# Kernel tuning notes

Measured on AMD Instinct MI355X. Metric: run time of the kernel, lower is better.

Reference implementation:

```python
import jax, jax.numpy as jnp
import numpy as np

H = 1024  # hidden_size
IN = 1024  # input_size
EPS = 1e-05


def _ln(v):
    # LayerNorm over last dim, no affine (gamma/beta applied by caller)
    c = v - v.mean(-1, keepdims=True)
    return c * jax.lax.rsqrt((c * c).mean(-1, keepdims=True) + EPS)


def setup_inputs() -> dict:
    key = jax.random.key(0)
    ks = jax.random.split(key, 12)
    stdv = 1.0 / np.sqrt(IN + 2 * H)
    u = lambda k, shape, s=stdv: jax.random.uniform(k, shape, jnp.float32, -s, s)
    bias = jnp.zeros((4 * H,), jnp.float32).at[:H].set(1.0)
    return {
        "input": jax.random.normal(ks[0], (512, 64, IN), jnp.float32),
        "hidden": jax.random.normal(ks[1], (64, H), jnp.float32),
        "cell": jax.random.normal(ks[2], (64, H), jnp.float32),
        "weight_ih": u(ks[3], (4 * H, IN)),
        "weight_hh": u(ks[4], (4 * H, H)),
        "weight_ch": u(ks[5], (3 * H,)),
        "bias": bias,
        "gamma_f": jax.random.uniform(ks[6], (H,), jnp.float32),
        "gamma_i": jax.random.uniform(ks[7], (H,), jnp.float32),
        "gamma_g": jax.random.uniform(ks[8], (H,), jnp.float32),
        "gamma_o": jax.random.uniform(ks[9], (H,), jnp.float32),
        "gamma_cell": jax.random.uniform(ks[10], (H,), jnp.float32),
        "beta_cell": jnp.zeros((H,), jnp.float32),
    }


def reference(input, hidden, cell, weight_ih, weight_hh, weight_ch, bias,
              gamma_f, gamma_i, gamma_g, gamma_o, gamma_cell, beta_cell):
    # input: [T, B, IN]; hidden/cell: [B, H]. Eval mode (dropout inactive).
    w_cf, w_ci, w_co = weight_ch[:H], weight_ch[H:2 * H], weight_ch[2 * H:]
    b_f, b_i, b_g, b_o = jnp.split(bias, 4)
    # Precompute input projections for all timesteps: [T, B, 4H]
    x_proj = jnp.einsum('tbi,gi->tbg', input, weight_ih)

    def step(carry, xp):
        h, c = carry
        gates = xp + h @ weight_hh.T  # [B, 4H]
        f_hat, i_hat, g_hat, o_hat = jnp.split(gates, 4, axis=-1)
        f = jax.nn.sigmoid(_ln(f_hat + w_cf * c) * gamma_f + b_f)
        i = jax.nn.sigmoid(_ln(i_hat + w_ci * c) * gamma_i + b_i)
        g = jnp.tanh(_ln(g_hat) * gamma_g + b_g)
        c_new = f * c + i * g
        c_ln = _ln(c_new) * gamma_cell + beta_cell
        o = jax.nn.sigmoid(_ln(o_hat + w_co * c_new) * gamma_o + b_o)
        h_new = o * jnp.tanh(c_ln)
        return (h_new, c_new), h_new

    (h_f, c_f), out = jax.lax.scan(step, (hidden, cell), x_proj)
    return out, h_f, c_f
```

## Files before the change

### kernel.cpp

```cpp
#include <hip/hip_runtime.h>

#define T_STEPS 512
#define BATCH   64
#define HID     1024
#define GDIM    4096
#define KDIM    2048
#define NGW     128
#define NSW     64
#define CWG     32
#define BHID    (BATCH * HID)

using short8  = __attribute__((ext_vector_type(8))) short;
using floatx4 = __attribute__((ext_vector_type(4))) float;
typedef unsigned long long u64;

__device__ inline unsigned short bf16_rne(float f) {
  union { float f; unsigned u; } x; x.f = f;
  unsigned r = x.u + 0x7FFFu + ((x.u >> 16) & 1u);
  return (unsigned short)(r >> 16);
}

__device__ inline float sigmoid_(float x) { return 1.0f / (1.0f + __expf(-x)); }
__device__ inline float tanh_(float x) {
  float e = __expf(-2.0f * fabsf(x));
  float r = (1.0f - e) / (1.0f + e);
  return copysignf(r, x);
}

#define LOAD4(dst, ptr) { float4 _t4 = *(const float4*)(ptr); \
  dst[0]=_t4.x; dst[1]=_t4.y; dst[2]=_t4.z; dst[3]=_t4.w; }

__device__ inline u64 ld_u64_mall(const void* p) {
  return __hip_atomic_load((const u64*)p, __ATOMIC_RELAXED, __HIP_MEMORY_SCOPE_AGENT);
}
__device__ inline void st_u64_mall(void* p, u64 v) {
  __hip_atomic_store((u64*)p, v, __ATOMIC_RELAXED, __HIP_MEMORY_SCOPE_AGENT);
}
__device__ inline void st_u32_mall(void* p, unsigned v) {
  __hip_atomic_store((unsigned*)p, v, __ATOMIC_RELAXED, __HIP_MEMORY_SCOPE_AGENT);
}
__device__ inline unsigned ld_u32_mall(const void* p) {
  return __hip_atomic_load((const unsigned*)p, __ATOMIC_RELAXED, __HIP_MEMORY_SCOPE_AGENT);
}
__device__ inline short8 ld_a16_mall(const unsigned short* p) {
  union { u64 q[2]; short8 v; } u;
  u.q[0] = ld_u64_mall(p);
  u.q[1] = ld_u64_mall(p + 4);
  return u.v;
}
__device__ inline void ld4f_mall(float* d, const float* p) {
  union { u64 q; float f[2]; } a, b;
  a.q = ld_u64_mall(p);
  b.q = ld_u64_mall(p + 2);
  d[0] = a.f[0]; d[1] = a.f[1]; d[2] = b.f[0]; d[3] = b.f[1];
}
__device__ inline void st4h_mall(unsigned short* p, float a, float b, float c, float d) {
  union { u64 q; unsigned short s[4]; } u;
  u.s[0] = bf16_rne(a); u.s[1] = bf16_rne(b); u.s[2] = bf16_rne(c); u.s[3] = bf16_rne(d);
  st_u64_mall(p, u.q);
}

__global__ __launch_bounds__(256) void cvt_w_kernel(
    const float* __restrict__ w_hh, const float* __restrict__ w_ih,
    unsigned short* __restrict__ wcat)
{
  int idx  = blockIdx.x * 256 + threadIdx.x;
  int base = idx * 4;
  int g = base >> 11;
  int k = base & 2047;
  const float* src = (k < 1024) ? (w_hh + (size_t)g * 1024 + k)
                                : (w_ih + (size_t)g * 1024 + (k - 1024));
  float a = src[0], b = src[1], c = src[2], d = src[3];
  uint2 v;
  v.x = (unsigned)bf16_rne(a) | ((unsigned)bf16_rne(b) << 16);
  v.y = (unsigned)bf16_rne(c) | ((unsigned)bf16_rne(d) << 16);
  *(uint2*)(wcat + base) = v;
}

__global__ __launch_bounds__(256) void cvt_x_kernel(
    const float* __restrict__ x, unsigned short* __restrict__ xall)
{
  size_t i = ((size_t)blockIdx.x * 256 + threadIdx.x) * 8;
  float4 a = *(const float4*)(x + i);
  float4 b = *(const float4*)(x + i + 4);
  union { unsigned short s[8]; uint4 v; } u;
  u.s[0] = bf16_rne(a.x); u.s[1] = bf16_rne(a.y); u.s[2] = bf16_rne(a.z); u.s[3] = bf16_rne(a.w);
  u.s[4] = bf16_rne(b.x); u.s[5] = bf16_rne(b.y); u.s[6] = bf16_rne(b.z); u.s[7] = bf16_rne(b.w);
  *(uint4*)(xall + i) = u.v;
}

__global__ __launch_bounds__(256) void init_kernel(
    const float* __restrict__ hidden, const float* __restrict__ x0,
    const float* __restrict__ cell,
    unsigned short* __restrict__ hdst, unsigned short* __restrict__ xdst,
    float* __restrict__ c_ws)
{
  const int b = blockIdx.x;
  const int j = threadIdx.x * 4;
  const size_t off = (size_t)b * HID + j;
  float4 h = *(const float4*)(hidden + off);
  float4 x = *(const float4*)(x0 + off);
  float4 c = *(const float4*)(cell + off);
  ushort4 hv, xv;
  hv.x = bf16_rne(h.x); hv.y = bf16_rne(h.y); hv.z = bf16_rne(h.z); hv.w = bf16_rne(h.w);
  xv.x = bf16_rne(x.x); xv.y = bf16_rne(x.y); xv.z = bf16_rne(x.z); xv.w = bf16_rne(x.w);
  *(ushort4*)(hdst + off) = hv;
  *(ushort4*)(xdst + off) = xv;
  *(float4*)(c_ws + off) = c;
}

template<int N>
__device__ inline void block_reduce(float* v, float* red, int tid) {
#pragma unroll
  for (int i = 0; i < N; ++i) {
    float x = v[i];
#pragma unroll
    for (int off = 32; off > 0; off >>= 1)
      x += __shfl_xor(x, off, 64);
    v[i] = x;
  }
  const int wave = tid >> 6;
  if ((tid & 63) == 0) {
#pragma unroll
    for (int i = 0; i < N; ++i) red[wave * N + i] = v[i];
  }
  __syncthreads();
#pragma unroll
  for (int i = 0; i < N; ++i)
    v[i] = red[i] + red[N + i] + red[2 * N + i] + red[3 * N + i];
}

#define MFMA16(a, b, c) __builtin_amdgcn_mfma_f32_16x16x32_bf16(a, b, c, 0, 0, 0)

template<int XALL>
__global__ __launch_bounds__(256, 1) void lstm_persist(
    const unsigned short* __restrict__ wcat,
    const float* __restrict__ input,
    const unsigned short* __restrict__ xA,
    unsigned short* __restrict__ xbuf,
    float* __restrict__ gates, float* __restrict__ c_ws,
    const float* __restrict__ w_ch, const float* __restrict__ bias,
    const float* __restrict__ gamma_f, const float* __restrict__ gamma_i,
    const float* __restrict__ gamma_g, const float* __restrict__ gamma_o,
    const float* __restrict__ gamma_c, const float* __restrict__ beta_c,
    float* __restrict__ out,
    unsigned short* __restrict__ hbuf,
    unsigned* __restrict__ syncp)
{
  __shared__ __align__(16) unsigned short smB[CWG * KDIM];
  __shared__ float sm[40];

  const int wg   = blockIdx.x;
  const int tid  = threadIdx.x;
  const int wave = tid >> 6;
  const int lane = tid & 63;
  const int quad = lane >> 4;
  const int l16  = lane & 15;

  unsigned* gflags = syncp;
  unsigned* hflags = syncp + NGW * 16;

  const floatx4 z = {0.f, 0.f, 0.f, 0.f};

  if (wg < NGW) {
    const int n0 = wg * CWG;
    for (int i = 0; i < 32; ++i) {
      int idx = wave * 32 + i;
      int t2 = idx >> 6, kc = idx & 63;
      short8 v = *(const short8*)(wcat + (size_t)(n0 + t2 * 16 + l16) * KDIM
                                  + kc * 32 + quad * 8);
      *(short8*)(smB + (size_t)idx * 512 + lane * 8) = v;
    }
    __syncthreads();

    const size_t rowoff = (size_t)(wave * 16 + l16) * HID + quad * 8;

    for (int t = 0; t < T_STEPS; ++t) {
      floatx4 x0e = z, x1e = z, x0o = z, x1o = z;
      if (XALL) {
        const unsigned short* ax = xA + (size_t)t * BHID + rowoff;
#pragma unroll
        for (int kc = 0; kc < 32; kc += 2) {
          short8 ae  = *(const short8*)(ax + kc * 32);
          short8 ao  = *(const short8*)(ax + (kc + 1) * 32);
          short8 b0e = *(const short8*)(smB + (size_t)(32 + kc) * 512 + lane * 8);
          short8 b1e = *(const short8*)(smB + (size_t)(96 + kc) * 512 + lane * 8);
          short8 b0o = *(const short8*)(smB + (size_t)(33 + kc) * 512 + lane * 8);
          short8 b1o = *(const short8*)(smB + (size_t)(97 + kc) * 512 + lane * 8);
          x0e = MFMA16(ae, b0e, x0e); x1e = MFMA16(ae, b1e, x1e);
          x0o = MFMA16(ao, b0o, x0o); x1o = MFMA16(ao, b1o, x1o);
        }
      }

      if (tid < NSW) {
        const unsigned* fp = hflags + tid * 16;
        while (ld_u32_mall(fp) < (unsigned)t) { }
      }
      __syncthreads();

      if (!XALL) {
#pragma unroll
        for (int kc = 0; kc < 32; kc += 2) {
          short8 ae  = ld_a16_mall(xA + rowoff + kc * 32);
          short8 ao  = ld_a16_mall(xA + rowoff + (kc + 1) * 32);
          short8 b0e = *(const short8*)(smB + (size_t)(32 + kc) * 512 + lane * 8);
          short8 b1e = *(const short8*)(smB + (size_t)(96 + kc) * 512 + lane * 8);
          short8 b0o = *(const short8*)(smB + (size_t)(33 + kc) * 512 + lane * 8);
          short8 b1o = *(const short8*)(smB + (size_t)(97 + kc) * 512 + lane * 8);
          x0e = MFMA16(ae, b0e, x0e); x1e = MFMA16(ae, b1e, x1e);
          x0o = MFMA16(ao, b0o, x0o); x1o = MFMA16(ao, b1o, x1o);
        }
      }

      short8 aH[32];
#pragma unroll
      for (int kc = 0; kc < 32; ++kc)
        aH[kc] = ld_a16_mall(hbuf + rowoff + kc * 32);

      floatx4 h0e = z, h1e = z, h0o = z, h1o = z;
#pragma unroll
      for (int kc = 0; kc < 32; kc += 2) {
        short8 b0e = *(const short8*)(smB + (size_t)kc * 512 + lane * 8);
        short8 b1e = *(const short8*)(smB + (size_t)(64 + kc) * 512 + lane * 8);
        short8 b0o = *(const short8*)(smB + (size_t)(kc + 1) * 512 + lane * 8);
        short8 b1o = *(const short8*)(smB + (size_t)(65 + kc) * 512 + lane * 8);
        h0e = MFMA16(aH[kc],     b0e, h0e); h1e = MFMA16(aH[kc],     b1e, h1e);
        h0o = MFMA16(aH[kc + 1], b0o, h0o); h1o = MFMA16(aH[kc + 1], b1o, h1o);
      }

#pragma unroll
      for (int r = 0; r < 4; ++r) {
        int m = wave * 16 + quad * 4 + r;
        float* gm = gates + (size_t)m * GDIM + n0 + l16;
        st_u32_mall(gm,      __float_as_uint((h0e[r] + h0o[r]) + (x0e[r] + x0o[r])));
        st_u32_mall(gm + 16, __float_as_uint((h1e[r] + h1o[r]) + (x1e[r] + x1o[r])));
      }
      asm volatile("s_waitcnt vmcnt(0)" ::: "memory");
      __syncthreads();
      if (tid == 0)
        st_u32_mall(gflags + wg * 16, (unsigned)(t + 1));
    }
  } else {
    const int b = wg - NGW;
    const int j = tid * 4;

    float cc[4], wcf[4], wci[4], wco[4];
    float gf4[4], gi4[4], gg4[4], go4[4], gc4[4], bc4[4];
    float bf4[4], bi4[4], bg4[4], bo4[4];
    LOAD4(cc,  c_ws + (size_t)b * HID + j);
    LOAD4(wcf, w_ch + j);
    LOAD4(wci, w_ch + HID + j);
    LOAD4(wco, w_ch + 2 * HID + j);
    LOAD4(gf4, gamma_f + j); LOAD4(gi4, gamma_i + j);
    LOAD4(gg4, gamma_g + j); LOAD4(go4, gamma_o + j);
    LOAD4(gc4, gamma_c + j); LOAD4(bc4, beta_c + j);
    LOAD4(bf4, bias + j);           LOAD4(bi4, bias + HID + j);
    LOAD4(bg4, bias + 2 * HID + j); LOAD4(bo4, bias + 3 * HID + j);
    const float invH = 1.0f / (float)HID;

    for (int t = 0; t < T_STEPS; ++t) {
      const int has_next = (t + 1 < T_STEPS);
      float4 xv;
      if (!XALL && has_next)
        xv = *(const float4*)(input + (size_t)(t + 1) * BHID + (size_t)b * HID + j);

      if (tid < NGW) {
        const unsigned* fp = gflags + tid * 16;
        while (ld_u32_mall(fp) < (unsigned)(t + 1)) { }
      }
      __syncthreads();

      float fh[4], ih[4], gh[4], oh[4];
      const float* grow = gates + (size_t)b * GDIM;
      ld4f_mall(fh, grow + j);
      ld4f_mall(ih, grow + HID + j);
      ld4f_mall(gh, grow + 2 * HID + j);
      ld4f_mall(oh, grow + 3 * HID + j);

      if (!XALL && has_next)
        st4h_mall(xbuf + (size_t)b * HID + j, xv.x, xv.y, xv.z, xv.w);

      float af[4], ai[4], ag[4];
      float s[6] = {0, 0, 0, 0, 0, 0};
#pragma unroll
      for (int r = 0; r < 4; ++r) {
        af[r] = fh[r] + wcf[r] * cc[r];
        ai[r] = ih[r] + wci[r] * cc[r];
        ag[r] = gh[r];
        s[0] += af[r]; s[1] += af[r] * af[r];
        s[2] += ai[r]; s[3] += ai[r] * ai[r];
        s[4] += ag[r]; s[5] += ag[r] * ag[r];
      }
      block_reduce<6>(s, sm, tid);
      float mu_f = s[0] * invH, is_f = rsqrtf(s[1] * invH - mu_f * mu_f + 1e-5f);
      float mu_i = s[2] * invH, is_i = rsqrtf(s[3] * invH - mu_i * mu_i + 1e-5f);
      float mu_g = s[4] * invH, is_g = rsqrtf(s[5] * invH - mu_g * mu_g + 1e-5f);

      float cn[4], ao[4];
      float s2[4] = {0, 0, 0, 0};
#pragma unroll
      for (int r = 0; r < 4; ++r) {
        float f = sigmoid_((af[r] - mu_f) * is_f * gf4[r] + bf4[r]);
        float i = sigmoid_((ai[r] - mu_i) * is_i * gi4[r] + bi4[r]);
        float g = tanh_((ag[r] - mu_g) * is_g * gg4[r] + bg4[r]);
        cn[r] = f * cc[r] + i * g;
        ao[r] = oh[r] + wco[r] * cn[r];
        s2[0] += cn[r]; s2[1] += cn[r] * cn[r];
        s2[2] += ao[r]; s2[3] += ao[r] * ao[r];
      }
#pragma unroll
      for (int r = 0; r < 4; ++r) cc[r] = cn[r];

      block_reduce<4>(s2, sm + 24, tid);
      float mu_c = s2[0] * invH, is_c = rsqrtf(s2[1] * invH - mu_c * mu_c + 1e-5f);
      float mu_o = s2[2] * invH, is_o = rsqrtf(s2[3] * invH - mu_o * mu_o + 1e-5f);

      float h4[4];
#pragma unroll
      for (int r = 0; r < 4; ++r) {
        float cl = (cn[r] - mu_c) * is_c * gc4[r] + bc4[r];
        float o  = sigmoid_((ao[r] - mu_o) * is_o * go4[r] + bo4[r]);
        h4[r] = o * tanh_(cl);
      }
      { float4 tt; tt.x = h4[0]; tt.y = h4[1]; tt.z = h4[2]; tt.w = h4[3];
        *(float4*)(out + (size_t)t * BHID + (size_t)b * HID + j) = tt; }
      st4h_mall(hbuf + (size_t)b * HID + j, h4[0], h4[1], h4[2], h4[3]);

      asm volatile("s_waitcnt vmcnt(0)" ::: "memory");
      __syncthreads();
      if (tid == 0)
        st_u32_mall(hflags + b * 16, (unsigned)(t + 1));
    }

    { float4 tt; tt.x = cc[0]; tt.y = cc[1]; tt.z = cc[2]; tt.w = cc[3];
      *(float4*)(c_ws + (size_t)b * HID + j) = tt; }
  }
}

extern "C" void kernel_launch(void* const* d_in, const int* in_sizes, int n_in,
                              void* d_out, int out_size, void* d_ws, size_t ws_size,
                              hipStream_t stream) {
  (void)in_sizes; (void)n_in; (void)out_size;
  const float* input   = (const float*)d_in[0];
  const float* hidden  = (const float*)d_in[1];
  const float* cell    = (const float*)d_in[2];
  const float* w_ih    = (const float*)d_in[3];
  const float* w_hh    = (const float*)d_in[4];
  const float* w_ch    = (const float*)d_in[5];
  const float* bias    = (const float*)d_in[6];
  const float* gamma_f = (const float*)d_in[7];
  const float* gamma_i = (const float*)d_in[8];
  const float* gamma_g = (const float*)d_in[9];
  const float* gamma_o = (const float*)d_in[10];
  const float* gamma_c = (const float*)d_in[11];
  const float* beta_c  = (const float*)d_in[12];
  float* out = (float*)d_out;

  const size_t SZ_WCAT = (size_t)GDIM * KDIM * sizeof(unsigned short);
  const size_t SZ_XALL = (size_t)T_STEPS * BHID * sizeof(unsigned short);
  const size_t SZ_BUF  = (size_t)BHID * sizeof(unsigned short);
  const size_t SZ_GATE = (size_t)BATCH * GDIM * sizeof(float);
  const size_t SZ_VEC  = (size_t)BHID * sizeof(float);
  const size_t SZ_FLAG = 16384;
  const size_t NEED_XALL = SZ_WCAT + SZ_XALL + SZ_BUF + SZ_GATE + SZ_VEC + SZ_FLAG;

  char* p = (char*)d_ws;
  unsigned short* wcat = (unsigned short*)p;  p += SZ_WCAT;
  const int xall = (ws_size >= NEED_XALL) ? 1 : 0;

  unsigned short *xA, *xbuf;
  if (xall) { xA = (unsigned short*)p; p += SZ_XALL; xbuf = xA; }
  else      { xA = (unsigned short*)p; p += SZ_BUF;  xbuf = xA; }
  unsigned short* hbuf = (unsigned short*)p;  p += SZ_BUF;
  float* gates = (float*)p;  p += SZ_GATE;
  float* c_ws  = (float*)p;  p += SZ_VEC;
  unsigned* syncp = (unsigned*)p;

  cvt_w_kernel<<<(GDIM * KDIM / 4) / 256, 256, 0, stream>>>(w_hh, w_ih, wcat);
  if (xall)
    cvt_x_kernel<<<((size_t)T_STEPS * BHID / 8) / 256, 256, 0, stream>>>(input, xA);
  init_kernel<<<BATCH, 256, 0, stream>>>(hidden, input, cell, hbuf, xA, c_ws);
  hipMemsetAsync(syncp, 0, SZ_FLAG, stream);

  if (xall)
    lstm_persist<1><<<NGW + NSW, 256, 0, stream>>>(
        wcat, input, xA, xbuf, gates, c_ws, w_ch, bias, gamma_f, gamma_i,
        gamma_g, gamma_o, gamma_c, beta_c, out, hbuf, syncp);
  else
    lstm_persist<0><<<NGW + NSW, 256, 0, stream>>>(
        wcat, input, xA, xbuf, gates, c_ws, w_ch, bias, gamma_f, gamma_i,
        gamma_g, gamma_o, gamma_c, beta_c, out, hbuf, syncp);

  const size_t OUT0 = (size_t)T_STEPS * BHID;
  hipMemcpyAsync(out + OUT0, out + (OUT0 - BHID),
                 (size_t)BHID * sizeof(float), hipMemcpyDeviceToDevice, stream);
  hipMemcpyAsync(out + OUT0 + BHID, c_ws,
                 (size_t)BHID * sizeof(float), hipMemcpyDeviceToDevice, stream);
}
```

Before: 7.245 ms.

## Use per-timestep hidden-state buffer pool and pack sync flags densely

Adds a mode where each timestep's bf16 hidden state goes to its own slot in a T-long pool, so the gate workgroups read h with ordinary cached loads instead of MALL-bypass loads. Reusing a single buffer forced uncached loads to avoid stale data. The sync flags are also packed contiguously instead of one per 64 bytes, which changes how the flag polling hits cache lines. The new mode needs extra workspace and falls back to the old modes when it is not available.

```diff
diff --git a/kernel.cpp b/kernel.cpp
--- a/kernel.cpp
+++ b/kernel.cpp
@@ -132,7 +132,7 @@
 
 #define MFMA16(a, b, c) __builtin_amdgcn_mfma_f32_16x16x32_bf16(a, b, c, 0, 0, 0)
 
-template<int XALL>
+template<int MODE>
 __global__ __launch_bounds__(256, 1) void lstm_persist(
     const unsigned short* __restrict__ wcat,
     const float* __restrict__ input,
@@ -144,7 +144,7 @@
     const float* __restrict__ gamma_g, const float* __restrict__ gamma_o,
     const float* __restrict__ gamma_c, const float* __restrict__ beta_c,
     float* __restrict__ out,
-    unsigned short* __restrict__ hbuf,
+    unsigned short* __restrict__ hA,
     unsigned* __restrict__ syncp)
 {
   __shared__ __align__(16) unsigned short smB[CWG * KDIM];
@@ -158,7 +158,7 @@
   const int l16  = lane & 15;
 
   unsigned* gflags = syncp;
-  unsigned* hflags = syncp + NGW * 16;
+  unsigned* hflags = syncp + 512;
 
   const floatx4 z = {0.f, 0.f, 0.f, 0.f};
 
@@ -177,7 +177,7 @@
 
     for (int t = 0; t < T_STEPS; ++t) {
       floatx4 x0e = z, x1e = z, x0o = z, x1o = z;
-      if (XALL) {
+      if (MODE >= 1) {
         const unsigned short* ax = xA + (size_t)t * BHID + rowoff;
 #pragma unroll
         for (int kc = 0; kc < 32; kc += 2) {
@@ -193,12 +193,12 @@
       }
 
       if (tid < NSW) {
-        const unsigned* fp = hflags + tid * 16;
+        const unsigned* fp = hflags + tid;
         while (ld_u32_mall(fp) < (unsigned)t) { }
       }
       __syncthreads();
 
-      if (!XALL) {
+      if (MODE == 0) {
 #pragma unroll
         for (int kc = 0; kc < 32; kc += 2) {
           short8 ae  = ld_a16_mall(xA + rowoff + kc * 32);
@@ -213,9 +213,16 @@
       }
 
       short8 aH[32];
-#pragma unroll
-      for (int kc = 0; kc < 32; ++kc)
-        aH[kc] = ld_a16_mall(hbuf + rowoff + kc * 32);
+      if (MODE == 2) {
+        const unsigned short* ah = hA + (size_t)t * BHID + rowoff;
+#pragma unroll
+        for (int kc = 0; kc < 32; ++kc)
+          aH[kc] = *(const short8*)(ah + kc * 32);
+      } else {
+#pragma unroll
+        for (int kc = 0; kc < 32; ++kc)
+          aH[kc] = ld_a16_mall(hA + rowoff + kc * 32);
+      }
 
       floatx4 h0e = z, h1e = z, h0o = z, h1o = z;
 #pragma unroll
@@ -238,7 +245,7 @@
       asm volatile("s_waitcnt vmcnt(0)" ::: "memory");
       __syncthreads();
       if (tid == 0)
-        st_u32_mall(gflags + wg * 16, (unsigned)(t + 1));
+        st_u32_mall(gflags + wg, (unsigned)(t + 1));
     }
   } else {
     const int b = wg - NGW;
@@ -261,11 +268,11 @@
     for (int t = 0; t < T_STEPS; ++t) {
       const int has_next = (t + 1 < T_STEPS);
       float4 xv;
-      if (!XALL && has_next)
+      if (MODE == 0 && has_next)
         xv = *(const float4*)(input + (size_t)(t + 1) * BHID + (size_t)b * HID + j);
 
       if (tid < NGW) {
-        const unsigned* fp = gflags + tid * 16;
+        const unsigned* fp = gflags + tid;
         while (ld_u32_mall(fp) < (unsigned)(t + 1)) { }
       }
       __syncthreads();
@@ -277,7 +284,7 @@
       ld4f_mall(gh, grow + 2 * HID + j);
       ld4f_mall(oh, grow + 3 * HID + j);
 
-      if (!XALL && has_next)
+      if (MODE == 0 && has_next)
         st4h_mall(xbuf + (size_t)b * HID + j, xv.x, xv.y, xv.z, xv.w);
 
       float af[4], ai[4], ag[4];
@@ -324,12 +331,17 @@
       }
       { float4 tt; tt.x = h4[0]; tt.y = h4[1]; tt.z = h4[2]; tt.w = h4[3];
         *(float4*)(out + (size_t)t * BHID + (size_t)b * HID + j) = tt; }
-      st4h_mall(hbuf + (size_t)b * HID + j, h4[0], h4[1], h4[2], h4[3]);
+      if (has_next) {
+        unsigned short* hd = (MODE == 2)
+            ? hA + (size_t)(t + 1) * BHID + (size_t)b * HID + j
+            : hA + (size_t)b * HID + j;
+        st4h_mall(hd, h4[0], h4[1], h4[2], h4[3]);
+      }
 
       asm volatile("s_waitcnt vmcnt(0)" ::: "memory");
       __syncthreads();
       if (tid == 0)
-        st_u32_mall(hflags + b * 16, (unsigned)(t + 1));
+        st_u32_mall(hflags + b, (unsigned)(t + 1));
     }
 
     { float4 tt; tt.x = cc[0]; tt.y = cc[1]; tt.z = cc[2]; tt.w = cc[3];
@@ -358,38 +370,49 @@
 
   const size_t SZ_WCAT = (size_t)GDIM * KDIM * sizeof(unsigned short);
   const size_t SZ_XALL = (size_t)T_STEPS * BHID * sizeof(unsigned short);
+  const size_t SZ_HPOOL= (size_t)T_STEPS * BHID * sizeof(unsigned short);
   const size_t SZ_BUF  = (size_t)BHID * sizeof(unsigned short);
   const size_t SZ_GATE = (size_t)BATCH * GDIM * sizeof(float);
   const size_t SZ_VEC  = (size_t)BHID * sizeof(float);
   const size_t SZ_FLAG = 16384;
-  const size_t NEED_XALL = SZ_WCAT + SZ_XALL + SZ_BUF + SZ_GATE + SZ_VEC + SZ_FLAG;
+  const size_t TAIL = SZ_GATE + SZ_VEC + SZ_FLAG;
+  const size_t NEED2 = SZ_WCAT + SZ_XALL + SZ_HPOOL + TAIL;
+  const size_t NEED1 = SZ_WCAT + SZ_XALL + SZ_BUF + TAIL;
 
   char* p = (char*)d_ws;
   unsigned short* wcat = (unsigned short*)p;  p += SZ_WCAT;
-  const int xall = (ws_size >= NEED_XALL) ? 1 : 0;
-
-  unsigned short *xA, *xbuf;
-  if (xall) { xA = (unsigned short*)p; p += SZ_XALL; xbuf = xA; }
-  else      { xA = (unsigned short*)p; p += SZ_BUF;  xbuf = xA; }
-  unsigned short* hbuf = (unsigned short*)p;  p += SZ_BUF;
+  int mode = (ws_size >= NEED2) ? 2 : (ws_size >= NEED1) ? 1 : 0;
+
+  unsigned short *xA, *xbuf, *hA;
+  if (mode >= 1) {
+    xA = (unsigned short*)p; p += SZ_XALL; xbuf = xA;
+    hA = (unsigned short*)p; p += (mode == 2) ? SZ_HPOOL : SZ_BUF;
+  } else {
+    xA = (unsigned short*)p; p += SZ_BUF;  xbuf = xA;
+    hA = (unsigned short*)p; p += SZ_BUF;
+  }
   float* gates = (float*)p;  p += SZ_GATE;
   float* c_ws  = (float*)p;  p += SZ_VEC;
   unsigned* syncp = (unsigned*)p;
 
   cvt_w_kernel<<<(GDIM * KDIM / 4) / 256, 256, 0, stream>>>(w_hh, w_ih, wcat);
-  if (xall)
+  if (mode >= 1)
     cvt_x_kernel<<<((size_t)T_STEPS * BHID / 8) / 256, 256, 0, stream>>>(input, xA);
-  init_kernel<<<BATCH, 256, 0, stream>>>(hidden, input, cell, hbuf, xA, c_ws);
+  init_kernel<<<BATCH, 256, 0, stream>>>(hidden, input, cell, hA, xA, c_ws);
   hipMemsetAsync(syncp, 0, SZ_FLAG, stream);
 
-  if (xall)
+  if (mode == 2)
+    lstm_persist<2><<<NGW + NSW, 256, 0, stream>>>(
+        wcat, input, xA, xbuf, gates, c_ws, w_ch, bias, gamma_f, gamma_i,
+        gamma_g, gamma_o, gamma_c, beta_c, out, hA, syncp);
+  else if (mode == 1)
     lstm_persist<1><<<NGW + NSW, 256, 0, stream>>>(
         wcat, input, xA, xbuf, gates, c_ws, w_ch, bias, gamma_f, gamma_i,
-        gamma_g, gamma_o, gamma_c, beta_c, out, hbuf, syncp);
+        gamma_g, gamma_o, gamma_c, beta_c, out, hA, syncp);
   else
     lstm_persist<0><<<NGW + NSW, 256, 0, stream>>>(
         wcat, input, xA, xbuf, gates, c_ws, w_ch, bias, gamma_f, gamma_i,
-        gamma_g, gamma_o, gamma_c, beta_c, out, hbuf, syncp);
+        gamma_g, gamma_o, gamma_c, beta_c, out, hA, syncp);
 
   const size_t OUT0 = (size_t)T_STEPS * BHID;
   hipMemcpyAsync(out + OUT0, out + (OUT0 - BHID),
```

New measurement: 7.010 ms. 1.03x faster.
